# Optimization experiments

Measured on AMD Instinct MI355X. Metric: run time of the kernel, lower is better.

## Reference

```python
import jax, jax.numpy as jnp
import numpy as np

B, HIST, PRED = 16, 336, 48
S = HIST + PRED                      # 384 = max_seq_length
H, NL, NH, FF = 768, 12, 12, 3072    # default BertConfig
SA_NH = 16                           # attention_heads arg for the extra SelfAttention
V = 40000                            # num_location_ids
NE = 8                               # num_experts
D_DAY, D_TIME, D_DOW, D_WD, D_LOC = 64, 64, 64, 32, 256
D_IN = D_DAY + D_TIME + D_DOW + D_WD + D_LOC + 1  # 481


def _ln(x, g, b, eps):
    m = jnp.mean(x, -1, keepdims=True)
    v = jnp.mean(jnp.square(x - m), -1, keepdims=True)
    return (x - m) * jax.lax.rsqrt(v + eps) * g + b


def _mha(x, qW, qb, kW, kb, vW, vb, nh):
    b_, s_, h_ = x.shape
    hd = h_ // nh
    q = (x @ qW + qb).reshape(b_, s_, nh, hd)
    k = (x @ kW + kb).reshape(b_, s_, nh, hd)
    v = (x @ vW + vb).reshape(b_, s_, nh, hd)
    scores = jnp.einsum('bqhd,bkhd->bhqk', q, k) / jnp.sqrt(jnp.float32(hd))
    probs = jax.nn.softmax(scores, axis=-1)
    return jnp.einsum('bhqk,bkhd->bqhd', probs, v).reshape(b_, s_, h_)


FLOAT_NAMES = ['day_emb', 'time_emb', 'dow_emb', 'wd_emb', 'loc_emb',
               'ln_in_g', 'ln_in_b', 'inp_W', 'inp_b', 'res_W', 'res_b',
               'sa_qW', 'sa_qb', 'sa_kW', 'sa_kb', 'sa_vW', 'sa_vb', 'sa_oW', 'sa_ob', 'sa_lng', 'sa_lnb',
               'pos_emb', 'tt_emb', 'be_lng', 'be_lnb',
               'bqW', 'bqb', 'bkW', 'bkb', 'bvW', 'bvb', 'boW', 'bob', 'balng', 'balnb',
               'bf1W', 'bf1b', 'bf2W', 'bf2b', 'bflng', 'bflnb',
               'moe_W', 'moe_b', 'gate_W', 'gate_b', 'out_W', 'out_b']


def _forward(floats, ints):
    (day_emb, time_emb, dow_emb, wd_emb, loc_emb,
     ln_in_g, ln_in_b, inp_W, inp_b, res_W, res_b,
     sa_qW, sa_qb, sa_kW, sa_kb, sa_vW, sa_vb, sa_oW, sa_ob, sa_lng, sa_lnb,
     pos_emb, tt_emb, be_lng, be_lnb,
     bqW, bqb, bkW, bkb, bvW, bvb, boW, bob, balng, balnb,
     bf1W, bf1b, bf2W, bf2b, bflng, bflnb,
     moe_W, moe_b, gate_W, gate_b, out_W, out_b) = floats
    isf, hloc, psf = ints

    def feat(f):
        return (day_emb[f[:, :, 0]], time_emb[f[:, :, 1]], dow_emb[f[:, :, 3]],
                wd_emb[f[:, :, 4]], f[:, :, 5].astype(jnp.float32)[..., None])
    hd_, ht_, hw_, hwd_, hdl = feat(isf)
    hist = jnp.concatenate([hd_, ht_, hw_, hwd_, hdl, loc_emb[hloc]], -1)
    fd_, ft_, fw_, fwd_, fdl = feat(psf)
    fut_loc = jnp.zeros((psf.shape[0], psf.shape[1], D_LOC), jnp.float32)  # unknown future locations
    fut = jnp.concatenate([fd_, ft_, fw_, fwd_, fdl, fut_loc], -1)
    x = jnp.concatenate([hist, fut], 1)            # [B,S,481]
    x = _ln(x, ln_in_g, ln_in_b, 1e-5)             # layer_norm on raw features (dropout = identity in eval)
    proj = x @ inp_W + inp_b                       # input_projection -> [B,S,768]
    res = x @ res_W + res_b                        # residual_fc -> [B,S,768]

    # extra SelfAttention block (16 heads) with post-LN residual
    ctx = _mha(proj, sa_qW, sa_qb, sa_kW, sa_kb, sa_vW, sa_vb, SA_NH)
    h = _ln(ctx @ sa_oW + sa_ob + proj, sa_lng, sa_lnb, 1e-5)

    # BERT encoder (inputs_embeds path): add position + token_type(0) embeddings, then 12 post-LN layers
    h = _ln(h + pos_emb[None] + tt_emb, be_lng, be_lnb, 1e-12)
    for i in range(NL):
        ctx = _mha(h, bqW[i], bqb[i], bkW[i], bkb[i], bvW[i], bvb[i], NH)
        a = _ln(ctx @ boW[i] + bob[i] + h, balng[i], balnb[i], 1e-12)
        ff = jax.nn.gelu(a @ bf1W[i] + bf1b[i], approximate=False) @ bf2W[i] + bf2b[i]
        h = _ln(ff + a, bflng[i], bflnb[i], 1e-12)

    # dense soft-MoE: every expert runs on every token, softmax-gated sum
    xf = h.reshape(-1, H)                                                 # [B*S, H]
    eo = jax.nn.gelu(jnp.einsum('nd,edh->neh', xf, moe_W) + moe_b[None], approximate=False)
    gp = jax.nn.softmax(xf @ gate_W + gate_b, axis=-1)                     # [B*S, E]
    moe_out = jnp.einsum('ne,neh->nh', gp, eo).reshape(h.shape)

    logits = (moe_out + res) @ out_W + out_b                               # [B,S,V]
    return logits[:, HIST:, :]                                             # predictions for future slots


def setup_inputs() -> dict:
    key = jax.random.key(0)
    ctr = [0]
    def nk():
        ctr[0] += 1
        return jax.random.fold_in(key, ctr[0])
    def nrm(shape, s=0.02):
        return jax.random.normal(nk(), shape, jnp.float32) * s
    p = {}
    p['input_seq_feature'] = jax.random.randint(nk(), (B, HIST, 6), 0, 2)
    p['historical_locations'] = jax.random.randint(nk(), (B, HIST), 0, V)
    p['predict_seq_feature'] = jax.random.randint(nk(), (B, PRED, 6), 0, 2)
    p['day_emb'] = nrm((75, D_DAY)); p['time_emb'] = nrm((48, D_TIME))
    p['dow_emb'] = nrm((7, D_DOW)); p['wd_emb'] = nrm((2, D_WD)); p['loc_emb'] = nrm((V, D_LOC))
    p['ln_in_g'] = jnp.ones((D_IN,), jnp.float32); p['ln_in_b'] = jnp.zeros((D_IN,), jnp.float32)
    p['inp_W'] = nrm((D_IN, H)); p['inp_b'] = jnp.zeros((H,), jnp.float32)
    p['res_W'] = nrm((D_IN, H)); p['res_b'] = jnp.zeros((H,), jnp.float32)
    for n in ['sa_qW', 'sa_kW', 'sa_vW', 'sa_oW']:
        p[n] = nrm((H, H))
    for n in ['sa_qb', 'sa_kb', 'sa_vb', 'sa_ob']:
        p[n] = jnp.zeros((H,), jnp.float32)
    p['sa_lng'] = jnp.ones((H,), jnp.float32); p['sa_lnb'] = jnp.zeros((H,), jnp.float32)
    p['pos_emb'] = nrm((S, H)); p['tt_emb'] = nrm((H,))
    p['be_lng'] = jnp.ones((H,), jnp.float32); p['be_lnb'] = jnp.zeros((H,), jnp.float32)
    for n in ['bqW', 'bkW', 'bvW', 'boW']:
        p[n] = nrm((NL, H, H))
    for n in ['bqb', 'bkb', 'bvb', 'bob']:
        p[n] = jnp.zeros((NL, H), jnp.float32)
    p['balng'] = jnp.ones((NL, H), jnp.float32); p['balnb'] = jnp.zeros((NL, H), jnp.float32)
    p['bf1W'] = nrm((NL, H, FF)); p['bf1b'] = jnp.zeros((NL, FF), jnp.float32)
    p['bf2W'] = nrm((NL, FF, H)); p['bf2b'] = jnp.zeros((NL, H), jnp.float32)
    p['bflng'] = jnp.ones((NL, H), jnp.float32); p['bflnb'] = jnp.zeros((NL, H), jnp.float32)
    p['moe_W'] = nrm((NE, H, H)); p['moe_b'] = jnp.zeros((NE, H), jnp.float32)
    p['gate_W'] = nrm((H, NE)); p['gate_b'] = jnp.zeros((NE,), jnp.float32)
    p['out_W'] = nrm((H, V)); p['out_b'] = jnp.zeros((V,), jnp.float32)
    return p


def reference(input_seq_feature, historical_locations, predict_seq_feature,
              day_emb, time_emb, dow_emb, wd_emb, loc_emb,
              ln_in_g, ln_in_b, inp_W, inp_b, res_W, res_b,
              sa_qW, sa_qb, sa_kW, sa_kb, sa_vW, sa_vb, sa_oW, sa_ob, sa_lng, sa_lnb,
              pos_emb, tt_emb, be_lng, be_lnb,
              bqW, bqb, bkW, bkb, bvW, bvb, boW, bob, balng, balnb,
              bf1W, bf1b, bf2W, bf2b, bflng, bflnb,
              moe_W, moe_b, gate_W, gate_b, out_W, out_b):
    floats = (day_emb, time_emb, dow_emb, wd_emb, loc_emb,
              ln_in_g, ln_in_b, inp_W, inp_b, res_W, res_b,
              sa_qW, sa_qb, sa_kW, sa_kb, sa_vW, sa_vb, sa_oW, sa_ob, sa_lng, sa_lnb,
              pos_emb, tt_emb, be_lng, be_lnb,
              bqW, bqb, bkW, bkb, bvW, bvb, boW, bob, balng, balnb,
              bf1W, bf1b, bf2W, bf2b, bflng, bflnb,
              moe_W, moe_b, gate_W, gate_b, out_W, out_b)
    ints = (input_seq_feature, historical_locations, predict_seq_feature)
    return _forward(floats, ints)
```

## Files before the change

### kernel.cpp

```cpp
#include <hip/hip_runtime.h>
#include <cstddef>
#include <math.h>

#define BB 16
#define HIST 336
#define PRED 48
#define SS 384
#define HH 768
#define NL 12
#define FF_ 3072
#define DIN 481
#define DINP 512
#define NE_ 8
#define VV 40000
#define VVP 40064

typedef __attribute__((ext_vector_type(8))) short short8;
typedef __attribute__((ext_vector_type(4))) float f32x4;
struct short4v { short x, y, z, w; };

__device__ __forceinline__ short f2bf(float f) {
    union { float f; unsigned u; } v; v.f = f;
    unsigned r = v.u + 0x7fff + ((v.u >> 16) & 1);
    return (short)(r >> 16);
}

using gvoid_t = const __attribute__((address_space(1))) void;
using svoid_t = __attribute__((address_space(3))) void;

template<int OP, bool SWZ>
__global__ __launch_bounds__(256)
void gemm_bf16(const short* __restrict__ A, const short* __restrict__ Bt,
               const float* __restrict__ bias, const float* __restrict__ bias2,
               const float* __restrict__ bias3,
               void* __restrict__ Cout, void* __restrict__ Cout2,
               int Kp, int M, int ldc)
{
    __shared__ short As[2][128 * 64];
    __shared__ short Bs[2][128 * 64];
    const int tid  = threadIdx.x;
    const int lane = tid & 63;
    const int w    = tid >> 6;
    const int wr = w >> 1, wc = w & 1;
    const int lrow = lane & 15, lgrp = lane >> 4;

    int bx = blockIdx.x, by = blockIdx.y;
    if (SWZ) {
        const int nwg = gridDim.x * gridDim.y;
        const int o = blockIdx.y * gridDim.x + blockIdx.x;
        const int xcd = o & 7, k = o >> 3;
        const int q = nwg >> 3, r = nwg & 7;
        const int nid = (xcd < r ? xcd * (q + 1) : r * (q + 1) + (xcd - r) * q) + k;
        bx = nid / gridDim.y;
        by = nid % gridDim.y;
    }
    const size_t rowBase = (size_t)by * 128;
    const size_t colBase = (size_t)bx * 128;

    f32x4 acc[4][4];
    #pragma unroll
    for (int i = 0; i < 4; ++i)
        #pragma unroll
        for (int j = 0; j < 4; ++j)
            acc[i][j] = f32x4{0.f, 0.f, 0.f, 0.f};

    const int nkt = Kp >> 6;

    auto stage = [&](int buf, int kt) {
        const short* Ab = A  + rowBase * Kp + (size_t)kt * 64;
        const short* Bb = Bt + colBase * Kp + (size_t)kt * 64;
        #pragma unroll
        for (int c = 0; c < 4; ++c) {
            const int sidx = (w * 4 + c) * 64 + lane;
            const int r = sidx >> 3, sl = sidx & 7;
            const int sseg = sl ^ (r & 7);
            __builtin_amdgcn_global_load_lds(
                (gvoid_t*)(Ab + (size_t)r * Kp + sseg * 8),
                (svoid_t*)&As[buf][(w * 4 + c) * 512], 16, 0, 0);
            __builtin_amdgcn_global_load_lds(
                (gvoid_t*)(Bb + (size_t)r * Kp + sseg * 8),
                (svoid_t*)&Bs[buf][(w * 4 + c) * 512], 16, 0, 0);
        }
    };

    int cur = 0;
    stage(0, 0);
    __syncthreads();
    for (int kt = 0; kt < nkt; ++kt) {
        if (kt + 1 < nkt) stage(cur ^ 1, kt + 1);
        const short* as = As[cur];
        const short* bs = Bs[cur];
        #pragma unroll
        for (int kk = 0; kk < 2; ++kk) {
            short8 aF[4], bF[4];
            #pragma unroll
            for (int mi = 0; mi < 4; ++mi) {
                const int r = wr * 64 + mi * 16 + lrow;
                const int seg = (kk * 4 + lgrp) ^ (r & 7);
                aF[mi] = *(const short8*)&as[r * 64 + seg * 8];
            }
            #pragma unroll
            for (int ni = 0; ni < 4; ++ni) {
                const int r = wc * 64 + ni * 16 + lrow;
                const int seg = (kk * 4 + lgrp) ^ (r & 7);
                bF[ni] = *(const short8*)&bs[r * 64 + seg * 8];
            }
            #pragma unroll
            for (int mi = 0; mi < 4; ++mi)
                #pragma unroll
                for (int ni = 0; ni < 4; ++ni)
                    acc[mi][ni] = __builtin_amdgcn_mfma_f32_16x16x32_bf16(
                        aF[mi], bF[ni], acc[mi][ni], 0, 0, 0);
        }
        __syncthreads();
        cur ^= 1;
    }

    #pragma unroll
    for (int mi = 0; mi < 4; ++mi) {
        #pragma unroll
        for (int ni = 0; ni < 4; ++ni) {
            const int col = (int)colBase + wc * 64 + ni * 16 + lrow;
            if (col >= M) continue;
            const float* bp = bias; int bc = col;
            if (bias2 && col >= HH) {
                if (col < 2 * HH) { bp = bias2; bc = col - HH; }
                else              { bp = bias3; bc = col - 2 * HH; }
            }
            const float bz = bp[bc];
            #pragma unroll
            for (int j = 0; j < 4; ++j) {
                const size_t row = rowBase + wr * 64 + mi * 16 + lgrp * 4 + j;
                float v = acc[mi][ni][j] + bz;
                if (OP == 1 || OP == 4)
                    v = 0.5f * v * (1.f + erff(v * 0.70710678118654752f));
                if (OP == 4 || OP == 5) ((short*)Cout)[row * ldc + col] = f2bf(v);
                else                    ((float*)Cout)[row * ldc + col] = v;
                if (OP == 6)            ((short*)Cout2)[row * ldc + col] = f2bf(v);
            }
        }
    }
}

template<int HD>
__global__ __launch_bounds__(256)
void attn_mfma(const short* __restrict__ Qg, const short* __restrict__ Kg,
               const short* __restrict__ Vg, short* __restrict__ Og,
               int nh, int ldq, int ldo, float scale)
{
    constexpr int NI = HD / 16;
    constexpr int SEGS = HD / 8;
    __shared__ short Qs[64 * 64];
    __shared__ short Ks[64 * 64];
    __shared__ short Vt[64 * 72];
    __shared__ short Ps[4][16 * 80];
    int idx = blockIdx.x;
    const int qt = idx % 6; idx /= 6;
    const int h = idx % nh; idx /= nh;
    const int b = idx;
    const int tid = threadIdx.x;
    const int lane = tid & 63;
    const int w = tid >> 6;
    const int lrow = lane & 15, lgrp = lane >> 4;

    const short* Qbase = Qg + ((size_t)(b * SS + qt * 64)) * ldq + h * HD;
    #pragma unroll
    for (int t = 0; t < 2; ++t) {
        const int i = tid + t * 256;
        const int r = i >> 3, sg = i & 7;
        short8 v = {0, 0, 0, 0, 0, 0, 0, 0};
        if (sg < SEGS) v = *(const short8*)(Qbase + (size_t)r * ldq + sg * 8);
        *(short8*)&Qs[r * 64 + (sg ^ (r & 7)) * 8] = v;
    }

    float m_[4], l_[4];
    f32x4 o_[NI];
    #pragma unroll
    for (int j = 0; j < 4; ++j) { m_[j] = -1e30f; l_[j] = 0.f; }
    #pragma unroll
    for (int ni = 0; ni < NI; ++ni) o_[ni] = f32x4{0.f, 0.f, 0.f, 0.f};

    for (int kt = 0; kt < 6; ++kt) {
        const short* Kb2 = Kg + ((size_t)(b * SS + kt * 64)) * ldq + h * HD;
        const short* Vb2 = Vg + ((size_t)(b * SS + kt * 64)) * ldq + h * HD;
        __syncthreads();
        #pragma unroll
        for (int c = 0; c < 2; ++c) {
            const int r = (w * 2 + c) * 8 + (lane >> 3);
            const int sg = (lane & 7) ^ (r & 7);
            __builtin_amdgcn_global_load_lds(
                (gvoid_t*)(Kb2 + (size_t)r * ldq + sg * 8),
                (svoid_t*)&Ks[(w * 2 + c) * 512], 16, 0, 0);
        }
        for (int i = tid; i < 64 * SEGS; i += 256) {
            const int k = i & 63, sg = i >> 6;
            short8 v = *(const short8*)(Vb2 + (size_t)k * ldq + sg * 8);
            #pragma unroll
            for (int j2 = 0; j2 < 8; ++j2)
                Vt[(sg * 8 + j2) * 72 + k] = v[j2];
        }
        __syncthreads();

        f32x4 s[4];
        #pragma unroll
        for (int ni = 0; ni < 4; ++ni) s[ni] = f32x4{0.f, 0.f, 0.f, 0.f};
        __builtin_amdgcn_s_setprio(1);
        #pragma unroll
        for (int kk = 0; kk < 2; ++kk) {
            const int ra = w * 16 + lrow;
            const short8 aF = *(const short8*)&Qs[ra * 64 + ((kk * 4 + lgrp) ^ (ra & 7)) * 8];
            #pragma unroll
            for (int ni = 0; ni < 4; ++ni) {
                const int rb = ni * 16 + lrow;
                const short8 bF = *(const short8*)&Ks[rb * 64 + ((kk * 4 + lgrp) ^ (rb & 7)) * 8];
                s[ni] = __builtin_amdgcn_mfma_f32_16x16x32_bf16(aF, bF, s[ni], 0, 0, 0);
            }
        }
        __builtin_amdgcn_s_setprio(0);
        #pragma unroll
        for (int ni = 0; ni < 4; ++ni)
            #pragma unroll
            for (int j = 0; j < 4; ++j) s[ni][j] *= scale;

        #pragma unroll
        for (int j = 0; j < 4; ++j) {
            float tm = fmaxf(fmaxf(s[0][j], s[1][j]), fmaxf(s[2][j], s[3][j]));
            #pragma unroll
            for (int d = 1; d < 16; d <<= 1) tm = fmaxf(tm, __shfl_xor(tm, d));
            const float mn = fmaxf(m_[j], tm);
            const float r2 = __expf(m_[j] - mn);
            float p[4], ps = 0.f;
            #pragma unroll
            for (int ni = 0; ni < 4; ++ni) { p[ni] = __expf(s[ni][j] - mn); ps += p[ni]; }
            #pragma unroll
            for (int d = 1; d < 16; d <<= 1) ps += __shfl_xor(ps, d);
            l_[j] = l_[j] * r2 + ps;
            m_[j] = mn;
            #pragma unroll
            for (int ni = 0; ni < NI; ++ni) o_[ni][j] *= r2;
            #pragma unroll
            for (int ni = 0; ni < 4; ++ni)
                Ps[w][(lgrp * 4 + j) * 80 + ni * 16 + lrow] = f2bf(p[ni]);
        }

        __builtin_amdgcn_s_setprio(1);
        #pragma unroll
        for (int kk = 0; kk < 2; ++kk) {
            const short8 aP = *(const short8*)&Ps[w][lrow * 80 + kk * 32 + lgrp * 8];
            #pragma unroll
            for (int ni = 0; ni < NI; ++ni) {
                const int d0 = ni * 16 + lrow;
                const short8 bV = *(const short8*)&Vt[d0 * 72 + (kk * 4 + lgrp) * 8];
                o_[ni] = __builtin_amdgcn_mfma_f32_16x16x32_bf16(aP, bV, o_[ni], 0, 0, 0);
            }
        }
        __builtin_amdgcn_s_setprio(0);
    }

    const size_t orow0 = (size_t)(b * SS + qt * 64 + w * 16);
    #pragma unroll
    for (int j = 0; j < 4; ++j) {
        const float inv = 1.f / l_[j];
        #pragma unroll
        for (int ni = 0; ni < NI; ++ni)
            Og[(orow0 + lgrp * 4 + j) * ldo + h * HD + ni * 16 + lrow] =
                f2bf(o_[ni][j] * inv);
    }
}

__global__ __launch_bounds__(256)
void transpose_cvt_b(const float* __restrict__ W, short* __restrict__ Wt,
                     int K, int M, int Kp, size_t sStride, size_t dStride)
{
    __shared__ float tile[32][33];
    const float* src = W + blockIdx.z * sStride;
    short* dst = Wt + blockIdx.z * dStride;
    const int m0 = blockIdx.x * 32, k0 = blockIdx.y * 32;
    const int tx = threadIdx.x, ty = threadIdx.y;
    #pragma unroll
    for (int i = 0; i < 4; ++i) {
        int k = k0 + ty + i * 8, m = m0 + tx;
        tile[ty + i * 8][tx] = (k < K && m < M) ? src[(size_t)k * M + m] : 0.f;
    }
    __syncthreads();
    #pragma unroll
    for (int i = 0; i < 4; ++i) {
        int m = m0 + ty + i * 8, k = k0 + tx;
        dst[(size_t)m * Kp + k] = f2bf(tile[tx][ty + i * 8]);
    }
}

__global__ __launch_bounds__(256)
void prep_layer_w(const float* __restrict__ bq, const float* __restrict__ bk,
                  const float* __restrict__ bv, const float* __restrict__ bo,
                  const float* __restrict__ f1, const float* __restrict__ f2,
                  short* __restrict__ qkvT, short* __restrict__ oT,
                  short* __restrict__ f1T, short* __restrict__ f2T)
{
    __shared__ float tile[32][33];
    int id = blockIdx.x;
    const float* src; short* dst; int K, M, tm, tk;
    if (id < 1728) {
        const int mat = id / 576, r = id % 576;
        src = mat == 0 ? bq : (mat == 1 ? bk : bv);
        dst = qkvT + (size_t)mat * HH * HH;
        K = HH; M = HH; tm = r % 24; tk = r / 24;
    } else if (id < 2304) {
        const int r = id - 1728;
        src = bo; dst = oT; K = HH; M = HH; tm = r % 24; tk = r / 24;
    } else if (id < 4608) {
        const int r = id - 2304;
        src = f1; dst = f1T; K = HH; M = FF_; tm = r % 96; tk = r / 96;
    } else {
        const int r = id - 4608;
        src = f2; dst = f2T; K = FF_; M = HH; tm = r % 24; tk = r / 24;
    }
    const int m0 = tm * 32, k0 = tk * 32;
    const int tx = threadIdx.x & 31, ty = threadIdx.x >> 5;
    #pragma unroll
    for (int i = 0; i < 4; ++i) {
        int k = k0 + ty + i * 8, m = m0 + tx;
        tile[ty + i * 8][tx] = src[(size_t)k * M + m];
    }
    __syncthreads();
    #pragma unroll
    for (int i = 0; i < 4; ++i) {
        int m = m0 + ty + i * 8, k = k0 + tx;
        dst[(size_t)m * K + k] = f2bf(tile[tx][ty + i * 8]);
    }
}

__global__ __launch_bounds__(256)
void cvt_bf16(const float* __restrict__ src, short* __restrict__ dst, int n4)
{
    int i = blockIdx.x * 256 + threadIdx.x;
    if (i >= n4) return;
    float4 v = reinterpret_cast<const float4*>(src)[i];
    short4v o = { f2bf(v.x), f2bf(v.y), f2bf(v.z), f2bf(v.w) };
    reinterpret_cast<short4v*>(dst)[i] = o;
}

__global__ __launch_bounds__(512)
void build_x(const int* __restrict__ isf, const int* __restrict__ hloc,
             const int* __restrict__ psf,
             const float* __restrict__ dayE, const float* __restrict__ timeE,
             const float* __restrict__ dowE, const float* __restrict__ wdE,
             const float* __restrict__ locE,
             const float* __restrict__ g, const float* __restrict__ b2,
             short* __restrict__ xb)
{
    const int tok = blockIdx.x;
    const int b = tok / SS, s = tok % SS;
    const int tid = threadIdx.x;
    __shared__ float red[512];
    const int* f;
    int loc = -1;
    if (s < HIST) { f = isf + (b * HIST + s) * 6; loc = hloc[b * HIST + s]; }
    else          { f = psf + (b * PRED + (s - HIST)) * 6; }
    float val = 0.f;
    if (tid < DIN) {
        int c = tid;
        if      (c < 64)  val = dayE[f[0] * 64 + c];
        else if (c < 128) val = timeE[f[1] * 64 + (c - 64)];
        else if (c < 192) val = dowE[f[3] * 64 + (c - 128)];
        else if (c < 224) val = wdE[f[4] * 32 + (c - 192)];
        else if (c == 224) val = (float)f[5];
        else val = (loc >= 0) ? locE[(size_t)loc * 256 + (c - 225)] : 0.f;
    }
    red[tid] = (tid < DIN) ? val : 0.f;
    __syncthreads();
    for (int o = 256; o > 0; o >>= 1) { if (tid < o) red[tid] += red[tid + o]; __syncthreads(); }
    float mean = red[0] / (float)DIN;
    __syncthreads();
    float d = (tid < DIN) ? (val - mean) : 0.f;
    red[tid] = d * d;
    __syncthreads();
    for (int o = 256; o > 0; o >>= 1) { if (tid < o) red[tid] += red[tid + o]; __syncthreads(); }
    float rstd = rsqrtf(red[0] / (float)DIN + 1e-5f);
    if (tid < DINP)
        xb[(size_t)tok * DINP + tid] =
            (tid < DIN) ? f2bf((val - mean) * rstd * g[tid] + b2[tid]) : (short)0;
}

__global__ __launch_bounds__(256)
void ln768w(float* __restrict__ out, short* __restrict__ outb,
            const float* __restrict__ in1, const float* __restrict__ in2,
            const float* __restrict__ pos, const float* __restrict__ tt,
            const float* __restrict__ g, const float* __restrict__ b2,
            float eps)
{
    const int w = threadIdx.x >> 6, lane = threadIdx.x & 63;
    const int row = blockIdx.x * 4 + w;
    const int s = row % SS;
    float4 v[3];
    float partial = 0.f;
    #pragma unroll
    for (int i = 0; i < 3; ++i) {
        const int c = i * 256 + lane * 4;
        float4 t = *(const float4*)&in1[(size_t)row * HH + c];
        if (in2) { float4 u = *(const float4*)&in2[(size_t)row * HH + c];
                   t.x += u.x; t.y += u.y; t.z += u.z; t.w += u.w; }
        if (pos) { float4 u = *(const float4*)&pos[(size_t)s * HH + c];
                   t.x += u.x; t.y += u.y; t.z += u.z; t.w += u.w; }
        if (tt)  { float4 u = *(const float4*)&tt[c];
                   t.x += u.x; t.y += u.y; t.z += u.z; t.w += u.w; }
        v[i] = t;
        partial += t.x + t.y + t.z + t.w;
    }
    #pragma unroll
    for (int d = 1; d < 64; d <<= 1) partial += __shfl_xor(partial, d);
    const float mean = partial * (1.f / 768.f);
    float p2 = 0.f;
    #pragma unroll
    for (int i = 0; i < 3; ++i) {
        float a = v[i].x - mean, b3 = v[i].y - mean, c3 = v[i].z - mean, d3 = v[i].w - mean;
        p2 += a * a + b3 * b3 + c3 * c3 + d3 * d3;
    }
    #pragma unroll
    for (int d = 1; d < 64; d <<= 1) p2 += __shfl_xor(p2, d);
    const float rstd = rsqrtf(p2 * (1.f / 768.f) + eps);
    #pragma unroll
    for (int i = 0; i < 3; ++i) {
        const int c = i * 256 + lane * 4;
        float4 gg = *(const float4*)&g[c];
        float4 bb = *(const float4*)&b2[c];
        float4 o;
        o.x = (v[i].x - mean) * rstd * gg.x + bb.x;
        o.y = (v[i].y - mean) * rstd * gg.y + bb.y;
        o.z = (v[i].z - mean) * rstd * gg.z + bb.z;
        o.w = (v[i].w - mean) * rstd * gg.w + bb.w;
        *(float4*)&out[(size_t)row * HH + c] = o;
        if (outb) {
            short4v ob = { f2bf(o.x), f2bf(o.y), f2bf(o.z), f2bf(o.w) };
            *(short4v*)&outb[(size_t)row * HH + c] = ob;
        }
    }
}

__global__ void gather_fut_f32(const float* __restrict__ src, float* __restrict__ dst, int D)
{
    const int r = blockIdx.x;
    const int b = r / PRED, t = r % PRED;
    const int srow = b * SS + HIST + t;
    for (int c = threadIdx.x; c < D; c += blockDim.x)
        dst[(size_t)r * D + c] = src[(size_t)srow * D + c];
}
__global__ void gather_fut_b16(const short* __restrict__ src, short* __restrict__ dst, int D)
{
    const int r = blockIdx.x;
    const int b = r / PRED, t = r % PRED;
    const int srow = b * SS + HIST + t;
    for (int c = threadIdx.x; c < D; c += blockDim.x)
        dst[(size_t)r * D + c] = src[(size_t)srow * D + c];
}

__global__ __launch_bounds__(256)
void gate_kernel(const float* __restrict__ Xf, const float* __restrict__ Wg,
                 const float* __restrict__ bg, float* __restrict__ out)
{
    const int row = blockIdx.x;
    const int tid = threadIdx.x;
    float a[NE_] = {};
    for (int k = tid; k < HH; k += 256) {
        float xv = Xf[(size_t)row * HH + k];
        #pragma unroll
        for (int e = 0; e < NE_; ++e) a[e] = fmaf(xv, Wg[k * NE_ + e], a[e]);
    }
    __shared__ float red[256];
    #pragma unroll
    for (int e = 0; e < NE_; ++e) {
        red[tid] = a[e]; __syncthreads();
        for (int o = 128; o > 0; o >>= 1) { if (tid < o) red[tid] += red[tid + o]; __syncthreads(); }
        if (tid == 0) out[(size_t)row * NE_ + e] = red[0] + bg[e];
        __syncthreads();
    }
}

__global__ void gate_softmax(float* __restrict__ gate)
{
    const int r = blockIdx.x * blockDim.x + threadIdx.x;
    if (r >= BB * PRED) return;
    float* p = gate + (size_t)r * NE_;
    float mx = p[0];
    for (int e = 1; e < NE_; ++e) mx = fmaxf(mx, p[e]);
    float s = 0.f, v[NE_];
    for (int e = 0; e < NE_; ++e) { v[e] = __expf(p[e] - mx); s += v[e]; }
    for (int e = 0; e < NE_; ++e) p[e] = v[e] / s;
}

__global__ __launch_bounds__(256)
void moe_reduce(const float* __restrict__ eo, const float* __restrict__ gp,
                float* __restrict__ futm)
{
    const int row = blockIdx.x;
    float g[NE_];
    #pragma unroll
    for (int e = 0; e < NE_; ++e) g[e] = gp[row * NE_ + e];
    for (int c = threadIdx.x; c < HH; c += 256) {
        float s = futm[(size_t)row * HH + c];
        #pragma unroll
        for (int e = 0; e < NE_; ++e)
            s = fmaf(g[e], eo[(size_t)row * (NE_ * HH) + e * HH + c], s);
        futm[(size_t)row * HH + c] = s;
    }
}

extern "C" void kernel_launch(void* const* d_in, const int* in_sizes, int n_in,
                              void* d_out, int out_size, void* d_ws, size_t ws_size,
                              hipStream_t stream)
{
    const int*   isf   = (const int*)  d_in[0];
    const int*   hloc  = (const int*)  d_in[1];
    const int*   psf   = (const int*)  d_in[2];
    const float* dayE  = (const float*)d_in[3];
    const float* timeE = (const float*)d_in[4];
    const float* dowE  = (const float*)d_in[5];
    const float* wdE   = (const float*)d_in[6];
    const float* locE  = (const float*)d_in[7];
    const float* ln_g  = (const float*)d_in[8];
    const float* ln_b  = (const float*)d_in[9];
    const float* inpW  = (const float*)d_in[10];
    const float* inpB  = (const float*)d_in[11];
    const float* resW  = (const float*)d_in[12];
    const float* resB  = (const float*)d_in[13];
    const float* saqW  = (const float*)d_in[14];
    const float* sakW  = (const float*)d_in[15];
    const float* savW  = (const float*)d_in[16];
    const float* saoW  = (const float*)d_in[17];
    const float* saqB  = (const float*)d_in[18];
    const float* sakB  = (const float*)d_in[19];
    const float* savB  = (const float*)d_in[20];
    const float* saoB  = (const float*)d_in[21];
    const float* salnG = (const float*)d_in[22];
    const float* salnB = (const float*)d_in[23];
    const float* posE  = (const float*)d_in[24];
    const float* ttE   = (const float*)d_in[25];
    const float* belnG = (const float*)d_in[26];
    const float* belnB = (const float*)d_in[27];
    const float* bqW   = (const float*)d_in[28];
    const float* bkW   = (const float*)d_in[29];
    const float* bvW   = (const float*)d_in[30];
    const float* boW   = (const float*)d_in[31];
    const float* bqB   = (const float*)d_in[32];
    const float* bkB   = (const float*)d_in[33];
    const float* bvB   = (const float*)d_in[34];
    const float* boB   = (const float*)d_in[35];
    const float* balnG = (const float*)d_in[36];
    const float* balnB = (const float*)d_in[37];
    const float* bf1W  = (const float*)d_in[38];
    const float* bf1B  = (const float*)d_in[39];
    const float* bf2W  = (const float*)d_in[40];
    const float* bf2B  = (const float*)d_in[41];
    const float* bflnG = (const float*)d_in[42];
    const float* bflnB = (const float*)d_in[43];
    const float* moeW  = (const float*)d_in[44];
    const float* moeB  = (const float*)d_in[45];
    const float* gateW = (const float*)d_in[46];
    const float* gateB = (const float*)d_in[47];
    const float* outW  = (const float*)d_in[48];
    const float* outB  = (const float*)d_in[49];

    const int N6 = BB * SS;
    const int NF = BB * PRED;

    char* base = (char*)d_ws;
    size_t off = 0;
    auto alloc = [&](size_t bytes) -> void* {
        void* p = base + off;
        off = (off + bytes + 255) & ~(size_t)255;
        return p;
    };

    short* xb     = (short*)alloc((size_t)N6 * DINP * 2);
    short* hb     = (short*)alloc((size_t)N6 * HH * 2);
    short* Ob     = (short*)alloc((size_t)N6 * HH * 2);
    short* QKVb   = (short*)alloc((size_t)N6 * 3 * HH * 2);
    float* Cb     = (float*)alloc((size_t)N6 * HH * 4);
    short* ffb    = (short*)alloc((size_t)N6 * FF_ * 2);
    float* Hh     = (float*)alloc((size_t)N6 * HH * 4);
    float* Abuf   = (float*)alloc((size_t)N6 * HH * 4);
    short* inpWt  = (short*)alloc((size_t)HH * DINP * 2);
    short* resWt  = (short*)alloc((size_t)HH * DINP * 2);
    short* saWt   = (short*)alloc((size_t)3 * HH * HH * 2);
    short* saoWt  = (short*)alloc((size_t)HH * HH * 2);
    short* lqkvWt = (short*)alloc((size_t)3 * HH * HH * 2);
    short* loWt   = (short*)alloc((size_t)HH * HH * 2);
    short* lf1Wt  = (short*)alloc((size_t)FF_ * HH * 2);
    short* lf2Wt  = (short*)alloc((size_t)HH * FF_ * 2);
    float* futh   = (float*)alloc((size_t)NF * HH * 4);
    float* futm   = (float*)alloc((size_t)NF * HH * 4);
    float* futg   = (float*)alloc((size_t)NF * NE_ * 4);

    short* outWt = QKVb;
    short* moeWt = outWt + (size_t)VVP * HH;
    short* futhb = moeWt + (size_t)NE_ * HH * HH;
    short* futxb = futhb + (size_t)NF * HH;
    short* futmb = futxb + (size_t)NF * DINP;

    build_x<<<N6, 512, 0, stream>>>(isf, hloc, psf, dayE, timeE, dowE, wdE, locE,
                                    ln_g, ln_b, xb);

    dim3 tb(32, 8);
    transpose_cvt_b<<<dim3(HH/32, DINP/32, 1), tb, 0, stream>>>(inpW, inpWt, DIN, HH, DINP, 0, 0);
    transpose_cvt_b<<<dim3(HH/32, DINP/32, 1), tb, 0, stream>>>(resW, resWt, DIN, HH, DINP, 0, 0);
    transpose_cvt_b<<<dim3(HH/32, HH/32, 1), tb, 0, stream>>>(saqW, saWt,                   HH, HH, HH, 0, 0);
    transpose_cvt_b<<<dim3(HH/32, HH/32, 1), tb, 0, stream>>>(sakW, saWt + (size_t)HH*HH,   HH, HH, HH, 0, 0);
    transpose_cvt_b<<<dim3(HH/32, HH/32, 1), tb, 0, stream>>>(savW, saWt + (size_t)2*HH*HH, HH, HH, HH, 0, 0);
    transpose_cvt_b<<<dim3(HH/32, HH/32, 1), tb, 0, stream>>>(saoW, saoWt, HH, HH, HH, 0, 0);

    gemm_bf16<6, false><<<dim3(HH/128, N6/128), 256, 0, stream>>>(
        xb, inpWt, inpB, nullptr, nullptr, Abuf, hb, DINP, HH, HH);

    gemm_bf16<5, false><<<dim3(3*HH/128, N6/128), 256, 0, stream>>>(
        hb, saWt, saqB, sakB, savB, QKVb, nullptr, HH, 3*HH, 3*HH);
    attn_mfma<48><<<BB*16*6, 256, 0, stream>>>(
        QKVb, QKVb + HH, QKVb + 2*HH, Ob, 16, 3*HH, HH, 1.f / sqrtf(48.f));
    gemm_bf16<0, false><<<dim3(HH/128, N6/128), 256, 0, stream>>>(
        Ob, saoWt, saoB, nullptr, nullptr, Cb, nullptr, HH, HH, HH);
    ln768w<<<N6/4, 256, 0, stream>>>(Hh, nullptr, Cb, Abuf, nullptr, nullptr,
                                     salnG, salnB, 1e-5f);

    ln768w<<<N6/4, 256, 0, stream>>>(Hh, hb, Hh, nullptr, posE, ttE,
                                     belnG, belnB, 1e-12f);

    for (int i = 0; i < NL; ++i) {
        const size_t wo = (size_t)i * HH * HH;
        const size_t bo = (size_t)i * HH;
        prep_layer_w<<<6912, 256, 0, stream>>>(
            bqW + wo, bkW + wo, bvW + wo, boW + wo,
            bf1W + (size_t)i * HH * FF_, bf2W + (size_t)i * FF_ * HH,
            lqkvWt, loWt, lf1Wt, lf2Wt);

        gemm_bf16<5, false><<<dim3(3*HH/128, N6/128), 256, 0, stream>>>(
            hb, lqkvWt, bqB + bo, bkB + bo, bvB + bo, QKVb, nullptr, HH, 3*HH, 3*HH);
        attn_mfma<64><<<BB*12*6, 256, 0, stream>>>(
            QKVb, QKVb + HH, QKVb + 2*HH, Ob, 12, 3*HH, HH, 0.125f);
        gemm_bf16<0, false><<<dim3(HH/128, N6/128), 256, 0, stream>>>(
            Ob, loWt, boB + bo, nullptr, nullptr, Cb, nullptr, HH, HH, HH);
        ln768w<<<N6/4, 256, 0, stream>>>(Abuf, hb, Cb, Hh, nullptr, nullptr,
                                         balnG + bo, balnB + bo, 1e-12f);
        gemm_bf16<4, false><<<dim3(FF_/128, N6/128), 256, 0, stream>>>(
            hb, lf1Wt, bf1B + (size_t)i * FF_, nullptr, nullptr, ffb, nullptr, HH, FF_, FF_);
        gemm_bf16<0, false><<<dim3(HH/128, N6/128), 256, 0, stream>>>(
            ffb, lf2Wt, bf2B + bo, nullptr, nullptr, Cb, nullptr, FF_, HH, HH);
        ln768w<<<N6/4, 256, 0, stream>>>(Hh, hb, Cb, Abuf, nullptr, nullptr,
                                         bflnG + bo, bflnB + bo, 1e-12f);
    }

    gather_fut_f32<<<NF, 256, 0, stream>>>(Hh, futh, HH);
    gather_fut_b16<<<NF, 256, 0, stream>>>(hb, futhb, HH);
    gather_fut_b16<<<NF, 256, 0, stream>>>(xb, futxb, DINP);

    gemm_bf16<0, false><<<dim3(HH/128, NF/128), 256, 0, stream>>>(
        futxb, resWt, resB, nullptr, nullptr, futm, nullptr, DINP, HH, HH);

    gate_kernel<<<NF, 256, 0, stream>>>(futh, gateW, gateB, futg);
    gate_softmax<<<3, 256, 0, stream>>>(futg);

    transpose_cvt_b<<<dim3(HH/32, HH/32, NE_), tb, 0, stream>>>(
        moeW, moeWt, HH, HH, HH, (size_t)HH*HH, (size_t)HH*HH);
    gemm_bf16<1, true><<<dim3(NE_*HH/128, NF/128), 256, 0, stream>>>(
        futhb, moeWt, moeB, nullptr, nullptr, Hh, nullptr, HH, NE_*HH, NE_*HH);
    moe_reduce<<<NF, 256, 0, stream>>>(Hh, futg, futm);

    {
        int n4 = (int)((size_t)NF * HH / 4);
        cvt_bf16<<<(n4 + 255) / 256, 256, 0, stream>>>(futm, futmb, n4);
    }
    transpose_cvt_b<<<dim3(VVP/32, HH/32, 1), tb, 0, stream>>>(
        outW, outWt, HH, VV, HH, 0, 0);
    gemm_bf16<0, true><<<dim3(VVP/128, NF/128), 256, 0, stream>>>(
        futmb, outWt, outB, nullptr, nullptr, (float*)d_out, nullptr, HH, VV, VV);
}
```

Baseline: 3.633 ms.

## Use triple-buffered K=32 GEMM pipeline with explicit vmcnt waits and setprio

Reworks the bf16 GEMM main loop to use three LDS buffers of K-depth 32 in place of two buffers of K-depth 64. Each iteration waits with a partial vmcnt and a single barrier, so loads run two stages ahead and the trailing __syncthreads goes away. The LDS swizzle is adapted to 4 segments per row, and the MFMA burst is raised in priority with s_setprio. This aims to hide global-to-LDS latency better and use less LDS, at the cost of more barriers per unit of K and reliance on exact vmcnt accounting for correctness.

```diff
diff --git a/kernel.cpp b/kernel.cpp
--- a/kernel.cpp
+++ b/kernel.cpp
@@ -36,8 +36,8 @@
                void* __restrict__ Cout, void* __restrict__ Cout2,
                int Kp, int M, int ldc)
 {
-    __shared__ short As[2][128 * 64];
-    __shared__ short Bs[2][128 * 64];
+    __shared__ short As[3][128 * 32];
+    __shared__ short Bs[3][128 * 32];
     const int tid  = threadIdx.x;
     const int lane = tid & 63;
     const int w    = tid >> 6;
@@ -64,56 +64,63 @@
         for (int j = 0; j < 4; ++j)
             acc[i][j] = f32x4{0.f, 0.f, 0.f, 0.f};
 
-    const int nkt = Kp >> 6;
+    const int nkt = Kp >> 5;
 
     auto stage = [&](int buf, int kt) {
-        const short* Ab = A  + rowBase * Kp + (size_t)kt * 64;
-        const short* Bb = Bt + colBase * Kp + (size_t)kt * 64;
-        #pragma unroll
-        for (int c = 0; c < 4; ++c) {
-            const int sidx = (w * 4 + c) * 64 + lane;
-            const int r = sidx >> 3, sl = sidx & 7;
-            const int sseg = sl ^ (r & 7);
+        const short* Ab = A  + rowBase * Kp + (size_t)kt * 32;
+        const short* Bb = Bt + colBase * Kp + (size_t)kt * 32;
+        #pragma unroll
+        for (int c = 0; c < 2; ++c) {
+            const int slot = c * 256 + w * 64 + lane;
+            const int r = slot >> 2, sl = slot & 3;
+            const int sseg = sl ^ (r & 3);
             __builtin_amdgcn_global_load_lds(
                 (gvoid_t*)(Ab + (size_t)r * Kp + sseg * 8),
-                (svoid_t*)&As[buf][(w * 4 + c) * 512], 16, 0, 0);
+                (svoid_t*)&As[buf][(c * 256 + w * 64) * 8], 16, 0, 0);
+        }
+        #pragma unroll
+        for (int c = 0; c < 2; ++c) {
+            const int slot = c * 256 + w * 64 + lane;
+            const int r = slot >> 2, sl = slot & 3;
+            const int sseg = sl ^ (r & 3);
             __builtin_amdgcn_global_load_lds(
                 (gvoid_t*)(Bb + (size_t)r * Kp + sseg * 8),
-                (svoid_t*)&Bs[buf][(w * 4 + c) * 512], 16, 0, 0);
+                (svoid_t*)&Bs[buf][(c * 256 + w * 64) * 8], 16, 0, 0);
         }
     };
 
-    int cur = 0;
     stage(0, 0);
-    __syncthreads();
+    if (nkt > 1) stage(1, 1);
+
     for (int kt = 0; kt < nkt; ++kt) {
-        if (kt + 1 < nkt) stage(cur ^ 1, kt + 1);
-        const short* as = As[cur];
-        const short* bs = Bs[cur];
-        #pragma unroll
-        for (int kk = 0; kk < 2; ++kk) {
-            short8 aF[4], bF[4];
-            #pragma unroll
-            for (int mi = 0; mi < 4; ++mi) {
-                const int r = wr * 64 + mi * 16 + lrow;
-                const int seg = (kk * 4 + lgrp) ^ (r & 7);
-                aF[mi] = *(const short8*)&as[r * 64 + seg * 8];
-            }
-            #pragma unroll
-            for (int ni = 0; ni < 4; ++ni) {
-                const int r = wc * 64 + ni * 16 + lrow;
-                const int seg = (kk * 4 + lgrp) ^ (r & 7);
-                bF[ni] = *(const short8*)&bs[r * 64 + seg * 8];
-            }
-            #pragma unroll
-            for (int mi = 0; mi < 4; ++mi)
-                #pragma unroll
-                for (int ni = 0; ni < 4; ++ni)
-                    acc[mi][ni] = __builtin_amdgcn_mfma_f32_16x16x32_bf16(
-                        aF[mi], bF[ni], acc[mi][ni], 0, 0, 0);
-        }
-        __syncthreads();
-        cur ^= 1;
+        if (kt + 1 < nkt) { asm volatile("s_waitcnt vmcnt(4)" ::: "memory"); }
+        else              { asm volatile("s_waitcnt vmcnt(0)" ::: "memory"); }
+        __builtin_amdgcn_s_barrier();
+        if (kt + 2 < nkt) stage((kt + 2) % 3, kt + 2);
+
+        const short* as = As[kt % 3];
+        const short* bs = Bs[kt % 3];
+        short8 aF[4], bF[4];
+        #pragma unroll
+        for (int mi = 0; mi < 4; ++mi) {
+            const int r = wr * 64 + mi * 16 + lrow;
+            const int seg = lgrp ^ (r & 3);
+            aF[mi] = *(const short8*)&as[r * 32 + seg * 8];
+        }
+        #pragma unroll
+        for (int ni = 0; ni < 4; ++ni) {
+            const int r = wc * 64 + ni * 16 + lrow;
+            const int seg = lgrp ^ (r & 3);
+            bF[ni] = *(const short8*)&bs[r * 32 + seg * 8];
+        }
+        __builtin_amdgcn_s_setprio(1);
+        #pragma unroll
+        for (int mi = 0; mi < 4; ++mi)
+            #pragma unroll
+            for (int ni = 0; ni < 4; ++ni)
+                acc[mi][ni] = __builtin_amdgcn_mfma_f32_16x16x32_bf16(
+                    aF[mi], bF[ni], acc[mi][ni], 0, 0, 0);
+        __builtin_amdgcn_s_setprio(0);
     }
 
     #pragma unroll
```

Measured after the change: 3.939 ms. +8.4%, slower.

## Keep residual stream in bf16, fuse double LayerNorm, batch weight prep upfront

Applied to the files above, without the earlier changes.

The residual stream, attention output projection and FFN2 outputs move from fp32 to bf16, so the LayerNorm kernels read and write half the bytes and the dual fp32/bf16 stores disappear. The self-attention LayerNorm and the BERT embedding LayerNorm (with position and token-type add) become one fused kernel. All 12 layers' weight transposes are issued as a single launch when workspace allows, replacing 12 separate launches inside the layer loop. In exchange the residual path is rounded to bf16 at every layer, which can add numerical error, and the upfront path uses a large extra workspace.

```diff
diff --git a/kernel.cpp b/kernel.cpp
--- a/kernel.cpp
+++ b/kernel.cpp
@@ -24,6 +24,10 @@
     unsigned r = v.u + 0x7fff + ((v.u >> 16) & 1);
     return (short)(r >> 16);
 }
+__device__ __forceinline__ float bf2f(short s) {
+    union { unsigned u; float f; } v; v.u = ((unsigned)(unsigned short)s) << 16;
+    return v.f;
+}
 
 using gvoid_t = const __attribute__((address_space(1))) void;
 using svoid_t = __attribute__((address_space(3))) void;
@@ -33,8 +37,7 @@
 void gemm_bf16(const short* __restrict__ A, const short* __restrict__ Bt,
                const float* __restrict__ bias, const float* __restrict__ bias2,
                const float* __restrict__ bias3,
-               void* __restrict__ Cout, void* __restrict__ Cout2,
-               int Kp, int M, int ldc)
+               void* __restrict__ Cout, int Kp, int M, int ldc)
 {
     __shared__ short As[2][128 * 64];
     __shared__ short Bs[2][128 * 64];
@@ -136,7 +139,6 @@
                     v = 0.5f * v * (1.f + erff(v * 0.70710678118654752f));
                 if (OP == 4 || OP == 5) ((short*)Cout)[row * ldc + col] = f2bf(v);
                 else                    ((float*)Cout)[row * ldc + col] = v;
-                if (OP == 6)            ((short*)Cout2)[row * ldc + col] = f2bf(v);
             }
         }
     }
@@ -291,29 +293,41 @@
 }
 
 __global__ __launch_bounds__(256)
-void prep_layer_w(const float* __restrict__ bq, const float* __restrict__ bk,
-                  const float* __restrict__ bv, const float* __restrict__ bo,
-                  const float* __restrict__ f1, const float* __restrict__ f2,
+void prep_layer_w(const float* __restrict__ bqA, const float* __restrict__ bkA,
+                  const float* __restrict__ bvA, const float* __restrict__ boA,
+                  const float* __restrict__ f1A, const float* __restrict__ f2A,
                   short* __restrict__ qkvT, short* __restrict__ oT,
                   short* __restrict__ f1T, short* __restrict__ f2T)
 {
     __shared__ float tile[32][33];
+    const size_t L = blockIdx.y;
+    const float* bq = bqA + L * HH * HH;
+    const float* bk = bkA + L * HH * HH;
+    const float* bv = bvA + L * HH * HH;
+    const float* bo = boA + L * HH * HH;
+    const float* f1 = f1A + L * HH * FF_;
+    const float* f2 = f2A + L * FF_ * HH;
+    short* qT = qkvT + L * 3 * HH * HH;
+    short* oT2 = oT + L * HH * HH;
+    short* f1T2 = f1T + L * HH * FF_;
+    short* f2T2 = f2T + L * FF_ * HH;
+
     int id = blockIdx.x;
     const float* src; short* dst; int K, M, tm, tk;
     if (id < 1728) {
         const int mat = id / 576, r = id % 576;
         src = mat == 0 ? bq : (mat == 1 ? bk : bv);
-        dst = qkvT + (size_t)mat * HH * HH;
+        dst = qT + (size_t)mat * HH * HH;
         K = HH; M = HH; tm = r % 24; tk = r / 24;
     } else if (id < 2304) {
         const int r = id - 1728;
-        src = bo; dst = oT; K = HH; M = HH; tm = r % 24; tk = r / 24;
+        src = bo; dst = oT2; K = HH; M = HH; tm = r % 24; tk = r / 24;
     } else if (id < 4608) {
         const int r = id - 2304;
-        src = f1; dst = f1T; K = HH; M = FF_; tm = r % 96; tk = r / 96;
+        src = f1; dst = f1T2; K = HH; M = FF_; tm = r % 96; tk = r / 96;
     } else {
         const int r = id - 4608;
-        src = f2; dst = f2T; K = FF_; M = HH; tm = r % 24; tk = r / 24;
+        src = f2; dst = f2T2; K = FF_; M = HH; tm = r % 24; tk = r / 24;
     }
     const int m0 = tm * 32, k0 = tk * 32;
     const int tx = threadIdx.x & 31, ty = threadIdx.x >> 5;
@@ -383,39 +397,32 @@
 }
 
 __global__ __launch_bounds__(256)
-void ln768w(float* __restrict__ out, short* __restrict__ outb,
-            const float* __restrict__ in1, const float* __restrict__ in2,
-            const float* __restrict__ pos, const float* __restrict__ tt,
+void ln768b(short* __restrict__ out, const short* __restrict__ in1,
+            const short* __restrict__ in2,
             const float* __restrict__ g, const float* __restrict__ b2,
             float eps)
 {
     const int w = threadIdx.x >> 6, lane = threadIdx.x & 63;
     const int row = blockIdx.x * 4 + w;
-    const int s = row % SS;
-    float4 v[3];
-    float partial = 0.f;
+    float t[12];
+    float sum = 0.f;
     #pragma unroll
     for (int i = 0; i < 3; ++i) {
         const int c = i * 256 + lane * 4;
-        float4 t = *(const float4*)&in1[(size_t)row * HH + c];
-        if (in2) { float4 u = *(const float4*)&in2[(size_t)row * HH + c];
-                   t.x += u.x; t.y += u.y; t.z += u.z; t.w += u.w; }
-        if (pos) { float4 u = *(const float4*)&pos[(size_t)s * HH + c];
-                   t.x += u.x; t.y += u.y; t.z += u.z; t.w += u.w; }
-        if (tt)  { float4 u = *(const float4*)&tt[c];
-                   t.x += u.x; t.y += u.y; t.z += u.z; t.w += u.w; }
-        v[i] = t;
-        partial += t.x + t.y + t.z + t.w;
-    }
-    #pragma unroll
-    for (int d = 1; d < 64; d <<= 1) partial += __shfl_xor(partial, d);
-    const float mean = partial * (1.f / 768.f);
+        short4v a = *(const short4v*)&in1[(size_t)row * HH + c];
+        short4v b = *(const short4v*)&in2[(size_t)row * HH + c];
+        t[i * 4 + 0] = bf2f(a.x) + bf2f(b.x);
+        t[i * 4 + 1] = bf2f(a.y) + bf2f(b.y);
+        t[i * 4 + 2] = bf2f(a.z) + bf2f(b.z);
+        t[i * 4 + 3] = bf2f(a.w) + bf2f(b.w);
+        sum += t[i*4] + t[i*4+1] + t[i*4+2] + t[i*4+3];
+    }
+    #pragma unroll
+    for (int d = 1; d < 64; d <<= 1) sum += __shfl_xor(sum, d);
+    const float mean = sum * (1.f / 768.f);
     float p2 = 0.f;
     #pragma unroll
-    for (int i = 0; i < 3; ++i) {
-        float a = v[i].x - mean, b3 = v[i].y - mean, c3 = v[i].z - mean, d3 = v[i].w - mean;
-        p2 += a * a + b3 * b3 + c3 * c3 + d3 * d3;
-    }
+    for (int i = 0; i < 12; ++i) { float d = t[i] - mean; p2 += d * d; }
     #pragma unroll
     for (int d = 1; d < 64; d <<= 1) p2 += __shfl_xor(p2, d);
     const float rstd = rsqrtf(p2 * (1.f / 768.f) + eps);
@@ -424,20 +431,83 @@
         const int c = i * 256 + lane * 4;
         float4 gg = *(const float4*)&g[c];
         float4 bb = *(const float4*)&b2[c];
-        float4 o;
-        o.x = (v[i].x - mean) * rstd * gg.x + bb.x;
-        o.y = (v[i].y - mean) * rstd * gg.y + bb.y;
-        o.z = (v[i].z - mean) * rstd * gg.z + bb.z;
-        o.w = (v[i].w - mean) * rstd * gg.w + bb.w;
-        *(float4*)&out[(size_t)row * HH + c] = o;
-        if (outb) {
-            short4v ob = { f2bf(o.x), f2bf(o.y), f2bf(o.z), f2bf(o.w) };
-            *(short4v*)&outb[(size_t)row * HH + c] = ob;
-        }
-    }
-}
-
-__global__ void gather_fut_f32(const float* __restrict__ src, float* __restrict__ dst, int D)
+        short4v ob = { f2bf((t[i*4+0] - mean) * rstd * gg.x + bb.x),
+                       f2bf((t[i*4+1] - mean) * rstd * gg.y + bb.y),
+                       f2bf((t[i*4+2] - mean) * rstd * gg.z + bb.z),
+                       f2bf((t[i*4+3] - mean) * rstd * gg.w + bb.w) };
+        *(short4v*)&out[(size_t)row * HH + c] = ob;
+    }
+}
+
+__global__ __launch_bounds__(256)
+void ln2_fused(short* __restrict__ out, const short* __restrict__ in1,
+               const short* __restrict__ in2,
+               const float* __restrict__ pos, const float* __restrict__ tt,
+               const float* __restrict__ g1, const float* __restrict__ b1,
+               const float* __restrict__ g2, const float* __restrict__ b2)
+{
+    const int w = threadIdx.x >> 6, lane = threadIdx.x & 63;
+    const int row = blockIdx.x * 4 + w;
+    const int s = row % SS;
+    float t[12];
+    float sum = 0.f;
+    #pragma unroll
+    for (int i = 0; i < 3; ++i) {
+        const int c = i * 256 + lane * 4;
+        short4v a = *(const short4v*)&in1[(size_t)row * HH + c];
+        short4v b = *(const short4v*)&in2[(size_t)row * HH + c];
+        t[i*4+0] = bf2f(a.x) + bf2f(b.x);
+        t[i*4+1] = bf2f(a.y) + bf2f(b.y);
+        t[i*4+2] = bf2f(a.z) + bf2f(b.z);
+        t[i*4+3] = bf2f(a.w) + bf2f(b.w);
+        sum += t[i*4] + t[i*4+1] + t[i*4+2] + t[i*4+3];
+    }
+    #pragma unroll
+    for (int d = 1; d < 64; d <<= 1) sum += __shfl_xor(sum, d);
+    float mean = sum * (1.f / 768.f);
+    float p2 = 0.f;
+    #pragma unroll
+    for (int i = 0; i < 12; ++i) { float d = t[i] - mean; p2 += d * d; }
+    #pragma unroll
+    for (int d = 1; d < 64; d <<= 1) p2 += __shfl_xor(p2, d);
+    float rstd = rsqrtf(p2 * (1.f / 768.f) + 1e-5f);
+    sum = 0.f;
+    #pragma unroll
+    for (int i = 0; i < 3; ++i) {
+        const int c = i * 256 + lane * 4;
+        float4 gg = *(const float4*)&g1[c];
+        float4 bb = *(const float4*)&b1[c];
+        float4 pp = *(const float4*)&pos[(size_t)s * HH + c];
+        float4 tz = *(const float4*)&tt[c];
+        t[i*4+0] = (t[i*4+0] - mean) * rstd * gg.x + bb.x + pp.x + tz.x;
+        t[i*4+1] = (t[i*4+1] - mean) * rstd * gg.y + bb.y + pp.y + tz.y;
+        t[i*4+2] = (t[i*4+2] - mean) * rstd * gg.z + bb.z + pp.z + tz.z;
+        t[i*4+3] = (t[i*4+3] - mean) * rstd * gg.w + bb.w + pp.w + tz.w;
+        sum += t[i*4] + t[i*4+1] + t[i*4+2] + t[i*4+3];
+    }
+    #pragma unroll
+    for (int d = 1; d < 64; d <<= 1) sum += __shfl_xor(sum, d);
+    mean = sum * (1.f / 768.f);
+    p2 = 0.f;
+    #pragma unroll
+    for (int i = 0; i < 12; ++i) { float d = t[i] - mean; p2 += d * d; }
+    #pragma unroll
+    for (int d = 1; d < 64; d <<= 1) p2 += __shfl_xor(p2, d);
+    rstd = rsqrtf(p2 * (1.f / 768.f) + 1e-12f);
+    #pragma unroll
+    for (int i = 0; i < 3; ++i) {
+        const int c = i * 256 + lane * 4;
+        float4 gg = *(const float4*)&g2[c];
+        float4 bb = *(const float4*)&b2[c];
+        short4v ob = { f2bf((t[i*4+0] - mean) * rstd * gg.x + bb.x),
+                       f2bf((t[i*4+1] - mean) * rstd * gg.y + bb.y),
+                       f2bf((t[i*4+2] - mean) * rstd * gg.z + bb.z),
+                       f2bf((t[i*4+3] - mean) * rstd * gg.w + bb.w) };
+        *(short4v*)&out[(size_t)row * HH + c] = ob;
+    }
+}
+
+__global__ void gather_fut_b16(const short* __restrict__ src, short* __restrict__ dst, int D)
 {
     const int r = blockIdx.x;
     const int b = r / PRED, t = r % PRED;
@@ -445,24 +515,16 @@
     for (int c = threadIdx.x; c < D; c += blockDim.x)
         dst[(size_t)r * D + c] = src[(size_t)srow * D + c];
 }
-__global__ void gather_fut_b16(const short* __restrict__ src, short* __restrict__ dst, int D)
-{
-    const int r = blockIdx.x;
-    const int b = r / PRED, t = r % PRED;
-    const int srow = b * SS + HIST + t;
-    for (int c = threadIdx.x; c < D; c += blockDim.x)
-        dst[(size_t)r * D + c] = src[(size_t)srow * D + c];
-}
-
-__global__ __launch_bounds__(256)
-void gate_kernel(const float* __restrict__ Xf, const float* __restrict__ Wg,
+
+__global__ __launch_bounds__(256)
+void gate_kernel(const short* __restrict__ Xb, const float* __restrict__ Wg,
                  const float* __restrict__ bg, float* __restrict__ out)
 {
     const int row = blockIdx.x;
     const int tid = threadIdx.x;
     float a[NE_] = {};
     for (int k = tid; k < HH; k += 256) {
-        float xv = Xf[(size_t)row * HH + k];
+        float xv = bf2f(Xb[(size_t)row * HH + k]);
         #pragma unroll
         for (int e = 0; e < NE_; ++e) a[e] = fmaf(xv, Wg[k * NE_ + e], a[e]);
     }
@@ -571,14 +633,14 @@
         return p;
     };
 
-    short* xb     = (short*)alloc((size_t)N6 * DINP * 2);
-    short* hb     = (short*)alloc((size_t)N6 * HH * 2);
-    short* Ob     = (short*)alloc((size_t)N6 * HH * 2);
-    short* QKVb   = (short*)alloc((size_t)N6 * 3 * HH * 2);
-    float* Cb     = (float*)alloc((size_t)N6 * HH * 4);
-    short* ffb    = (short*)alloc((size_t)N6 * FF_ * 2);
-    float* Hh     = (float*)alloc((size_t)N6 * HH * 4);
-    float* Abuf   = (float*)alloc((size_t)N6 * HH * 4);
+    short* xb   = (short*)alloc((size_t)N6 * DINP * 2);
+    short* pb   = (short*)alloc((size_t)N6 * HH * 2);
+    short* ab   = (short*)alloc((size_t)N6 * HH * 2);
+    short* Ob   = (short*)alloc((size_t)N6 * HH * 2);
+    short* hcur = (short*)alloc((size_t)N6 * HH * 2);
+    short* QKVb = (short*)alloc((size_t)N6 * 3 * HH * 2);
+    short* C16  = (short*)alloc((size_t)N6 * HH * 2);
+    short* ffb  = (short*)alloc((size_t)N6 * FF_ * 2);
     short* inpWt  = (short*)alloc((size_t)HH * DINP * 2);
     short* resWt  = (short*)alloc((size_t)HH * DINP * 2);
     short* saWt   = (short*)alloc((size_t)3 * HH * HH * 2);
@@ -587,15 +649,26 @@
     short* loWt   = (short*)alloc((size_t)HH * HH * 2);
     short* lf1Wt  = (short*)alloc((size_t)FF_ * HH * 2);
     short* lf2Wt  = (short*)alloc((size_t)HH * FF_ * 2);
-    float* futh   = (float*)alloc((size_t)NF * HH * 4);
     float* futm   = (float*)alloc((size_t)NF * HH * 4);
     float* futg   = (float*)alloc((size_t)NF * NE_ * 4);
+
+    const size_t perL = ((size_t)3*HH*HH + (size_t)HH*HH + (size_t)HH*FF_ + (size_t)FF_*HH) * 2;
+    short* LqkvA = nullptr; short* LoA = nullptr; short* Lf1A = nullptr; short* Lf2A = nullptr;
+    bool upfront = false;
+    if (ws_size > off + 12 * perL + (32u << 20)) {
+        LqkvA = (short*)alloc((size_t)12 * 3 * HH * HH * 2);
+        LoA   = (short*)alloc((size_t)12 * HH * HH * 2);
+        Lf1A  = (short*)alloc((size_t)12 * HH * FF_ * 2);
+        Lf2A  = (short*)alloc((size_t)12 * FF_ * HH * 2);
+        upfront = true;
+    }
 
     short* outWt = QKVb;
     short* moeWt = outWt + (size_t)VVP * HH;
     short* futhb = moeWt + (size_t)NE_ * HH * HH;
     short* futxb = futhb + (size_t)NF * HH;
     short* futmb = futxb + (size_t)NF * DINP;
+    float* eoF   = (float*)pb;
 
     build_x<<<N6, 512, 0, stream>>>(isf, hloc, psf, dayE, timeE, dowE, wdE, locE,
                                     ln_g, ln_b, xb);
@@ -607,61 +680,66 @@
     transpose_cvt_b<<<dim3(HH/32, HH/32, 1), tb, 0, stream>>>(sakW, saWt + (size_t)HH*HH,   HH, HH, HH, 0, 0);
     transpose_cvt_b<<<dim3(HH/32, HH/32, 1), tb, 0, stream>>>(savW, saWt + (size_t)2*HH*HH, HH, HH, HH, 0, 0);
     transpose_cvt_b<<<dim3(HH/32, HH/32, 1), tb, 0, stream>>>(saoW, saoWt, HH, HH, HH, 0, 0);
-
-    gemm_bf16<6, false><<<dim3(HH/128, N6/128), 256, 0, stream>>>(
-        xb, inpWt, inpB, nullptr, nullptr, Abuf, hb, DINP, HH, HH);
+    if (upfront)
+        prep_layer_w<<<dim3(6912, 12), 256, 0, stream>>>(
+            bqW, bkW, bvW, boW, bf1W, bf2W, LqkvA, LoA, Lf1A, Lf2A);
+
+    gemm_bf16<5, false><<<dim3(HH/128, N6/128), 256, 0, stream>>>(
+        xb, inpWt, inpB, nullptr, nullptr, pb, DINP, HH, HH);
 
     gemm_bf16<5, false><<<dim3(3*HH/128, N6/128), 256, 0, stream>>>(
-        hb, saWt, saqB, sakB, savB, QKVb, nullptr, HH, 3*HH, 3*HH);
+        pb, saWt, saqB, sakB, savB, QKVb, HH, 3*HH, 3*HH);
     attn_mfma<48><<<BB*16*6, 256, 0, stream>>>(
         QKVb, QKVb + HH, QKVb + 2*HH, Ob, 16, 3*HH, HH, 1.f / sqrtf(48.f));
-    gemm_bf16<0, false><<<dim3(HH/128, N6/128), 256, 0, stream>>>(
-        Ob, saoWt, saoB, nullptr, nullptr, Cb, nullptr, HH, HH, HH);
-    ln768w<<<N6/4, 256, 0, stream>>>(Hh, nullptr, Cb, Abuf, nullptr, nullptr,
-                                     salnG, salnB, 1e-5f);
-
-    ln768w<<<N6/4, 256, 0, stream>>>(Hh, hb, Hh, nullptr, posE, ttE,
-                                     belnG, belnB, 1e-12f);
+    gemm_bf16<5, false><<<dim3(HH/128, N6/128), 256, 0, stream>>>(
+        Ob, saoWt, saoB, nullptr, nullptr, C16, HH, HH, HH);
+    ln2_fused<<<N6/4, 256, 0, stream>>>(hcur, C16, pb, posE, ttE,
+                                        salnG, salnB, belnG, belnB);
 
     for (int i = 0; i < NL; ++i) {
-        const size_t wo = (size_t)i * HH * HH;
         const size_t bo = (size_t)i * HH;
-        prep_layer_w<<<6912, 256, 0, stream>>>(
-            bqW + wo, bkW + wo, bvW + wo, boW + wo,
-            bf1W + (size_t)i * HH * FF_, bf2W + (size_t)i * FF_ * HH,
-            lqkvWt, loWt, lf1Wt, lf2Wt);
+        const short* wQ; const short* wO; const short* wF1; const short* wF2;
+        if (upfront) {
+            wQ  = LqkvA + (size_t)i * 3 * HH * HH;
+            wO  = LoA   + (size_t)i * HH * HH;
+            wF1 = Lf1A  + (size_t)i * HH * FF_;
+            wF2 = Lf2A  + (size_t)i * FF_ * HH;
+        } else {
+            prep_layer_w<<<dim3(6912, 1), 256, 0, stream>>>(
+                bqW + (size_t)i*HH*HH, bkW + (size_t)i*HH*HH, bvW + (size_t)i*HH*HH,
+                boW + (size_t)i*HH*HH, bf1W + (size_t)i*HH*FF_, bf2W + (size_t)i*FF_*HH,
+                lqkvWt, loWt, lf1Wt, lf2Wt);
+            wQ = lqkvWt; wO = loWt; wF1 = lf1Wt; wF2 = lf2Wt;
+        }
 
         gemm_bf16<5, false><<<dim3(3*HH/128, N6/128), 256, 0, stream>>>(
-            hb, lqkvWt, bqB + bo, bkB + bo, bvB + bo, QKVb, nullptr, HH, 3*HH, 3*HH);
+            hcur, wQ, bqB + bo, bkB + bo, bvB + bo, QKVb, HH, 3*HH, 3*HH);
         attn_mfma<64><<<BB*12*6, 256, 0, stream>>>(
             QKVb, QKVb + HH, QKVb + 2*HH, Ob, 12, 3*HH, HH, 0.125f);
-        gemm_bf16<0, false><<<dim3(HH/128, N6/128), 256, 0, stream>>>(
-            Ob, loWt, boB + bo, nullptr, nullptr, Cb, nullptr, HH, HH, HH);
-        ln768w<<<N6/4, 256, 0, stream>>>(Abuf, hb, Cb, Hh, nullptr, nullptr,
-                                         balnG + bo, balnB + bo, 1e-12f);
+        gemm_bf16<5, false><<<dim3(HH/128, N6/128), 256, 0, stream>>>(
+            Ob, wO, boB + bo, nullptr, nullptr, C16, HH, HH, HH);
+        ln768b<<<N6/4, 256, 0, stream>>>(ab, C16, hcur, balnG + bo, balnB + bo, 1e-12f);
         gemm_bf16<4, false><<<dim3(FF_/128, N6/128), 256, 0, stream>>>(
-            hb, lf1Wt, bf1B + (size_t)i * FF_, nullptr, nullptr, ffb, nullptr, HH, FF_, FF_);
-        gemm_bf16<0, false><<<dim3(HH/128, N6/128), 256, 0, stream>>>(
-            ffb, lf2Wt, bf2B + bo, nullptr, nullptr, Cb, nullptr, FF_, HH, HH);
-        ln768w<<<N6/4, 256, 0, stream>>>(Hh, hb, Cb, Abuf, nullptr, nullptr,
-                                         bflnG + bo, bflnB + bo, 1e-12f);
-    }
-
-    gather_fut_f32<<<NF, 256, 0, stream>>>(Hh, futh, HH);
-    gather_fut_b16<<<NF, 256, 0, stream>>>(hb, futhb, HH);
+            ab, wF1, bf1B + (size_t)i * FF_, nullptr, nullptr, ffb, HH, FF_, FF_);
+        gemm_bf16<5, false><<<dim3(HH/128, N6/128), 256, 0, stream>>>(
+            ffb, wF2, bf2B + bo, nullptr, nullptr, C16, FF_, HH, HH);
+        ln768b<<<N6/4, 256, 0, stream>>>(hcur, C16, ab, bflnG + bo, bflnB + bo, 1e-12f);
+    }
+
+    gather_fut_b16<<<NF, 256, 0, stream>>>(hcur, futhb, HH);
     gather_fut_b16<<<NF, 256, 0, stream>>>(xb, futxb, DINP);
 
     gemm_bf16<0, false><<<dim3(HH/128, NF/128), 256, 0, stream>>>(
-        futxb, resWt, resB, nullptr, nullptr, futm, nullptr, DINP, HH, HH);
-
-    gate_kernel<<<NF, 256, 0, stream>>>(futh, gateW, gateB, futg);
+        futxb, resWt, resB, nullptr, nullptr, futm, DINP, HH, HH);
+
+    gate_kernel<<<NF, 256, 0, stream>>>(futhb, gateW, gateB, futg);
     gate_softmax<<<3, 256, 0, stream>>>(futg);
 
     transpose_cvt_b<<<dim3(HH/32, HH/32, NE_), tb, 0, stream>>>(
         moeW, moeWt, HH, HH, HH, (size_t)HH*HH, (size_t)HH*HH);
     gemm_bf16<1, true><<<dim3(NE_*HH/128, NF/128), 256, 0, stream>>>(
-        futhb, moeWt, moeB, nullptr, nullptr, Hh, nullptr, HH, NE_*HH, NE_*HH);
-    moe_reduce<<<NF, 256, 0, stream>>>(Hh, futg, futm);
+        futhb, moeWt, moeB, nullptr, nullptr, eoF, HH, NE_*HH, NE_*HH);
+    moe_reduce<<<NF, 256, 0, stream>>>(eoF, futg, futm);
 
     {
         int n4 = (int)((size_t)NF * HH / 4);
@@ -670,5 +748,5 @@
     transpose_cvt_b<<<dim3(VVP/32, HH/32, 1), tb, 0, stream>>>(
         outW, outWt, HH, VV, HH, 0, 0);
     gemm_bf16<0, true><<<dim3(VVP/128, NF/128), 256, 0, stream>>>(
-        futmb, outWt, outB, nullptr, nullptr, (float*)d_out, nullptr, HH, VV, VV);
-}
+        futmb, outWt, outB, nullptr, nullptr, (float*)d_out, HH, VV, VV);
+}
```

New measurement: 3.663 ms. About the same (+0.8%).
